# Kernel tuning notes

Measured on AMD Instinct MI355X. Metric: run time of the kernel, lower is better.

## Reference

```python
import jax, jax.numpy as jnp
import numpy as np

N_HEADS = 8
N_POINTS = 4
LN_EPS = 1e-5


def _ln(x, g, b):
    m = jnp.mean(x, -1, keepdims=True)
    v = jnp.mean((x - m) ** 2, -1, keepdims=True)
    return (x - m) * jax.lax.rsqrt(v + LN_EPS) * g + b


def _mha(q, k, v, wq, bq, wk, bk, wv, bv, wo, bo):
    B, Lq, C = q.shape
    Dh = C // N_HEADS
    Q = (q @ wq.T + bq).reshape(B, Lq, N_HEADS, Dh)
    K = (k @ wk.T + bk).reshape(B, -1, N_HEADS, Dh)
    V = (v @ wv.T + bv).reshape(B, -1, N_HEADS, Dh)
    s = jnp.einsum('bqhd,bkhd->bhqk', Q, K) * (1.0 / float(np.sqrt(Dh)))
    a = jax.nn.softmax(s, -1)
    o = jnp.einsum('bhqk,bkhd->bqhd', a, V).reshape(B, Lq, C)
    return o @ wo.T + bo


def _ref_points(h, w, L):
    ry = jnp.linspace(0.5, h - 0.5, h) / h
    rx = jnp.linspace(0.5, w - 0.5, w) / w
    gy, gx = jnp.meshgrid(ry, rx, indexing='ij')
    ref = jnp.stack([gx.reshape(-1), gy.reshape(-1)], -1)[None]  # (1, h*w, 2)
    return jnp.broadcast_to(ref[:, :, None, :], (1, h * w, L, 2))


def _deform_core(value, shapes, starts, loc, aw):
    # value: (B, Len_in, H, Dh); loc: (B, Lq, H, L, P, 2); aw: (B, Lq, H, L, P)
    B, _, H, Dh = value.shape
    Lq, P = loc.shape[1], loc.shape[4]
    out = jnp.zeros((B, H, Lq, Dh), value.dtype)
    for l in range(shapes.shape[0]):
        Hl, Wl = int(shapes[l, 0]), int(shapes[l, 1])
        s = int(starts[l])
        v = value[:, s:s + Hl * Wl].transpose(0, 2, 1, 3)  # (B, H, Hl*Wl, Dh)
        # grid_sample(align_corners=False, padding_mode='zeros') pixel coords
        xl = loc[:, :, :, l, :, 0] * Wl - 0.5  # (B, Lq, H, P)
        yl = loc[:, :, :, l, :, 1] * Hl - 0.5
        x0 = jnp.floor(xl); y0 = jnp.floor(yl)
        fx = xl - x0; fy = yl - y0
        x0 = x0.astype(jnp.int32); y0 = y0.astype(jnp.int32)
        acc = jnp.zeros((B, H, Lq, P, Dh), value.dtype)
        for dy, dx in ((0, 0), (0, 1), (1, 0), (1, 1)):
            xi = x0 + dx; yi = y0 + dy
            wgt = (fx if dx else 1.0 - fx) * (fy if dy else 1.0 - fy)
            valid = ((xi >= 0) & (xi < Wl) & (yi >= 0) & (yi < Hl)).astype(value.dtype)
            idx = (jnp.clip(yi, 0, Hl - 1) * Wl + jnp.clip(xi, 0, Wl - 1))
            idx = idx.transpose(0, 2, 1, 3).reshape(B, H, Lq * P)
            g = jnp.take_along_axis(v, idx[..., None], axis=2).reshape(B, H, Lq, P, Dh)
            acc = acc + g * (wgt * valid).transpose(0, 2, 1, 3)[..., None]
        out = out + jnp.einsum('bhqpd,bqhp->bhqd', acc, aw[:, :, :, l])
    return out.transpose(0, 2, 1, 3).reshape(B, Lq, H * Dh)


def reference(tgt, query_pos, src, wq, bq, wk, bk, wv, bv, wo, bo, ln2_g, ln2_b,
              w_off, b_off, w_attn, b_attn, w_val, b_val, w_cout, b_cout,
              ln1_g, ln1_b, w1, b1, w2, b2, ln3_g, ln3_b,
              src_spatial_shapes, level_start_index, h, w):
    shapes = np.asarray(src_spatial_shapes)
    starts = np.asarray(level_start_index)
    h = int(h); w = int(w)
    L = shapes.shape[0]
    B, Lq, C = tgt.shape
    Dh = C // N_HEADS
    # --- self attention (post-LN residual) ---
    q = tgt + query_pos
    t2 = _mha(q, q, tgt, wq, bq, wk, bk, wv, bv, wo, bo)
    t = _ln(tgt + t2, ln2_g, ln2_b)
    # --- MSDeformAttn cross attention ---
    qc = t + query_pos
    value = (src @ w_val.T + b_val).reshape(B, -1, N_HEADS, Dh)
    off = (qc @ w_off.T + b_off).reshape(B, Lq, N_HEADS, L, N_POINTS, 2)
    aw = (qc @ w_attn.T + b_attn).reshape(B, Lq, N_HEADS, L * N_POINTS)
    aw = jax.nn.softmax(aw, -1).reshape(B, Lq, N_HEADS, L, N_POINTS)
    norm = jnp.stack([shapes[:, 1].astype(np.float32), shapes[:, 0].astype(np.float32)], -1)  # (L,2): (W,H)
    rp = _ref_points(h, w, L)  # (1, Lq, L, 2)
    loc = rp[:, :, None, :, None, :] + off / norm[None, None, None, :, None, :]
    samp = _deform_core(value, shapes, starts, loc, aw)
    t2 = samp @ w_cout.T + b_cout
    t = _ln(t + t2, ln1_g, ln1_b)
    # --- FFN ---
    t2 = jax.nn.relu(t @ w1.T + b1) @ w2.T + b2
    t = _ln(t + t2, ln3_g, ln3_b)
    return t


def setup_inputs() -> dict:
    key = jax.random.key(0)
    B, C, L, P, dff = 2, 256, 4, 4, 1024
    h = w = 48
    shapes = np.array([[48, 48], [24, 24], [12, 12], [6, 6]], np.int32)
    starts = np.array([0, 2304, 2880, 3024], np.int32)
    Len_in = 3060
    Lq = h * w
    ks = iter(jax.random.split(key, 40))
    def rn(shape, s=0.02):
        return jax.random.normal(next(ks), shape, jnp.float32) * s
    return dict(
        tgt=rn((B, Lq, C), 1.0), query_pos=rn((B, Lq, C), 1.0), src=rn((B, Len_in, C), 1.0),
        wq=rn((C, C)), bq=rn((C,)), wk=rn((C, C)), bk=rn((C,)), wv=rn((C, C)), bv=rn((C,)),
        wo=rn((C, C)), bo=rn((C,)),
        ln2_g=jnp.ones((C,)), ln2_b=jnp.zeros((C,)),
        w_off=rn((N_HEADS * L * P * 2, C)), b_off=rn((N_HEADS * L * P * 2,)),
        w_attn=rn((N_HEADS * L * P, C)), b_attn=rn((N_HEADS * L * P,)),
        w_val=rn((C, C)), b_val=rn((C,)), w_cout=rn((C, C)), b_cout=rn((C,)),
        ln1_g=jnp.ones((C,)), ln1_b=jnp.zeros((C,)),
        w1=rn((dff, C)), b1=rn((dff,)), w2=rn((C, dff)), b2=rn((C,)),
        ln3_g=jnp.ones((C,)), ln3_b=jnp.zeros((C,)),
        src_spatial_shapes=shapes, level_start_index=starts, h=h, w=w)
```

## Files before the change

kernel.cpp:

```cpp
#include <hip/hip_runtime.h>
#include <hip/hip_bf16.h>
#include <math.h>

typedef __hip_bfloat16 bf16;
typedef __attribute__((ext_vector_type(8))) short short8;
typedef __attribute__((ext_vector_type(4))) short short4v;
typedef __attribute__((ext_vector_type(4))) float f32x4;

static constexpr int B   = 2;
static constexpr int LQ  = 2304;
static constexpr int C   = 256;
static constexpr int NH  = 8;
static constexpr int DH  = 32;
static constexpr int NL  = 4;
static constexpr int NP  = 4;
static constexpr int LEN = 3060;
static constexpr int DFF = 1024;
static constexpr int MQ  = B * LQ;
static constexpr int MV  = B * LEN;
static constexpr int SZ1 = MQ * C;

#define MFMA16(a, b, c) __builtin_amdgcn_mfma_f32_16x16x32_bf16(a, b, c, 0, 0, 0)

__device__ __forceinline__ float ldf(const void* p, size_t i, int bf) {
  return bf ? __bfloat162float(((const bf16*)p)[i]) : ((const float*)p)[i];
}
__device__ __forceinline__ short fl2s(float v) {
  bf16 h = __float2bfloat16(v);
  return *(short*)&h;
}
__device__ __forceinline__ short fl2s_fast(float v) {
  union { float f; unsigned u; } x; x.f = v;
  return (short)((x.u + 0x8000u) >> 16);
}
__device__ __forceinline__ float s2fl(short s) {
  return __bfloat162float(*(bf16*)&s);
}
__device__ __forceinline__ int wire_is_bf16(const unsigned* gprobe) {
  return gprobe[0] == 0x3F803F80u;
}
__device__ __forceinline__ short8 add2bf(short8 a, short8 b) {
  short8 r;
#pragma unroll
  for (int j = 0; j < 8; ++j) r[j] = fl2s(s2fl(a[j]) + s2fl(b[j]));
  return r;
}

static constexpr int CVN = 20;
__device__ const int g_cvt_cnt[CVN] = {
  65536, 65536, 256, 256, 65536, 256, 65536, 256,
  65536, 32768, 256, 128, 65536, 256, 65536, 256,
  262144, 1024, 262144, 256};
__device__ const int g_cvt_off[CVN] = {
  0, 65536, 131072, 131328, 131584, 197120, 197376, 262912,
  263168, 328704, 361472, 361728, 361856, 427392, 427648, 493184,
  493440, 755584, 756608, 1018752};
static constexpr int CV_WQ = 0, CV_WK = 65536, CV_BQ = 131072, CV_BK = 131328;
static constexpr int CV_WV = 131584, CV_BV = 197120;
static constexpr int CV_WO = 197376, CV_BO = 262912;
static constexpr int CV_WOFF = 263168, CV_WATTN = 328704;
static constexpr int CV_BOFF = 361472, CV_BATTN = 361728;
static constexpr int CV_WVAL = 361856, CV_BVAL = 427392;
static constexpr int CV_WCOUT = 427648, CV_BCOUT = 493184;
static constexpr int CV_W1 = 493440, CV_B1 = 755584;
static constexpr int CV_W2 = 756608, CV_B2 = 1018752;
static constexpr int CV_TOTAL = 1019008;

struct CvtArgs { const void* p[22]; };

__global__ __launch_bounds__(256) void prep_all(CvtArgs a, const void* __restrict__ qpos,
                                                short* __restrict__ cvt,
                                                short* __restrict__ tgt16,
                                                short* __restrict__ q16,
                                                short* __restrict__ src16,
                                                const unsigned* __restrict__ gprobe) {
  if (wire_is_bf16(gprobe)) return;
  const int seg = blockIdx.y;
  const int cnt = (seg < 20) ? g_cvt_cnt[seg] : (seg == 20 ? SZ1 : MV * C);
  const int stride = gridDim.x * 256;
  for (int i = blockIdx.x * 256 + threadIdx.x; i < cnt; i += stride) {
    if (seg < 20) {
      cvt[g_cvt_off[seg] + i] = fl2s(((const float*)a.p[seg])[i]);
    } else if (seg == 20) {
      float t = ((const float*)a.p[20])[i];
      tgt16[i] = fl2s(t);
      q16[i] = fl2s(t + ((const float*)qpos)[i]);
    } else {
      src16[i] = fl2s(((const float*)a.p[21])[i]);
    }
  }
}

struct GemmJob {
  int Xmode;
  const short* Xbf; const void* Xwire; const void* Xwire2;
  const short* Wcvt; const short* bcvt;
  const void* Wwire; const void* bwire;
  void* Y;
  int M, N, K, ldY, col0, relu, out_mode, nblk_x;
  float qscale;
};
struct GemmBatch { GemmJob j[4]; int start[5]; int njobs; };

template <int MR>
__global__ __launch_bounds__(256) void gemm_mfma(GemmBatch nb,
                                                 const unsigned* __restrict__ gprobe) {
  constexpr int MT = MR / 64;
  const int fl = wire_is_bf16(gprobe);
  int id = blockIdx.x;
  int jj = 0;
  while (jj + 1 < nb.njobs && id >= nb.start[jj + 1]) ++jj;
  const GemmJob jb = nb.j[jj];
  const bool qcf = (jb.Xmode == 4) && fl;
  const short* Xsel = jb.Xbf;
  if ((jb.Xmode == 2 || jb.Xmode == 3) && fl) Xsel = (const short*)jb.Xwire;
  const short* Wsel = fl ? (const short*)jb.Wwire : jb.Wcvt;
  const short* bsel = fl ? (const short*)jb.bwire : jb.bcvt;
  const int local = id - nb.start[jj];
  const int bx = local % jb.nblk_x;
  const int by = local / jb.nblk_x;
  const int M = jb.M, N = jb.N, K = jb.K;

  __shared__ short Xs[MR][72];
  __shared__ short Ws[64][72];
  const int tid = threadIdx.x;
  const int wave = tid >> 6, lane = tid & 63;
  const int quad = lane >> 4, l16 = lane & 15;
  const int m0 = bx * MR, n0 = by * 64;
  f32x4 acc[MT][4];
#pragma unroll
  for (int mt = 0; mt < MT; ++mt)
#pragma unroll
    for (int nt = 0; nt < 4; ++nt) acc[mt][nt] = f32x4{0.f, 0.f, 0.f, 0.f};

  const int xrow = (MR == 128) ? (tid >> 1) : (tid >> 2);
  const int xcol = (MR == 128) ? ((tid & 1) * 32) : ((tid & 3) * 16);
  constexpr int XU = (MR == 128) ? 4 : 2;
  const int wrow = tid >> 2;
  const int wcol = (tid & 3) * 16;
  int xr = m0 + xrow; if (xr >= M) xr = M - 1;
  const short* xp = qcf ? nullptr : (Xsel + (size_t)xr * K);
  const short* tp = qcf ? ((const short*)jb.Xwire + (size_t)xr * K) : nullptr;
  const short* pp = qcf ? ((const short*)jb.Xwire2 + (size_t)xr * K) : nullptr;
  const short* wp = Wsel + (size_t)(n0 + wrow) * K;

  for (int k0 = 0; k0 < K; k0 += 64) {
    if (qcf) {
#pragma unroll
      for (int u = 0; u < XU; ++u) {
        short8 t8 = *(const short8*)(tp + k0 + xcol + u * 8);
        short8 p8 = *(const short8*)(pp + k0 + xcol + u * 8);
        *(short8*)&Xs[xrow][xcol + u * 8] = add2bf(t8, p8);
      }
    } else {
#pragma unroll
      for (int u = 0; u < XU; ++u)
        *(short8*)&Xs[xrow][xcol + u * 8] = *(const short8*)(xp + k0 + xcol + u * 8);
    }
    *(short8*)&Ws[wrow][wcol]     = *(const short8*)(wp + k0 + wcol);
    *(short8*)&Ws[wrow][wcol + 8] = *(const short8*)(wp + k0 + wcol + 8);
    __syncthreads();
#pragma unroll
    for (int kc = 0; kc < 2; ++kc) {
#pragma unroll
      for (int mt = 0; mt < MT; ++mt) {
        short8 a = *(const short8*)&Xs[wave * (16 * MT) + mt * 16 + l16][kc * 32 + quad * 8];
#pragma unroll
        for (int nt = 0; nt < 4; ++nt) {
          short8 b = *(const short8*)&Ws[nt * 16 + l16][kc * 32 + quad * 8];
          acc[mt][nt] = MFMA16(a, b, acc[mt][nt]);
        }
      }
    }
    __syncthreads();
  }

  if (jb.out_mode == 2) {
#pragma unroll
    for (int mt = 0; mt < MT; ++mt) {
      const int mbase = m0 + wave * (16 * MT) + mt * 16 + quad * 4;
      const int b = mbase / LQ;
      const int qb_ = mbase - b * LQ;
#pragma unroll
      for (int nt = 0; nt < 4; ++nt) {
        const int n = n0 + nt * 16 + l16;
        const float bv = s2fl(bsel[n]);
        short4v v4;
#pragma unroll
        for (int r = 0; r < 4; ++r) v4[r] = fl2s(acc[mt][nt][r] + bv);
        *(short4v*)((short*)jb.Y + (size_t)(b * 256 + n) * LQ + qb_) = v4;
      }
    }
    return;
  }
#pragma unroll
  for (int mt = 0; mt < MT; ++mt)
#pragma unroll
    for (int nt = 0; nt < 4; ++nt) {
      const int n = n0 + nt * 16 + l16;
      const float bv = s2fl(bsel[n]);
#pragma unroll
      for (int r = 0; r < 4; ++r) {
        const int m = m0 + wave * (16 * MT) + mt * 16 + quad * 4 + r;
        if (m < M) {
          float v = (acc[mt][nt][r] + bv) * jb.qscale;
          if (jb.relu) v = fmaxf(v, 0.f);
          if (jb.out_mode == 1)
            ((short*)jb.Y)[(size_t)m * jb.ldY + jb.col0 + n] = fl2s(v);
          else
            ((float*)jb.Y)[(size_t)m * jb.ldY + jb.col0 + n] = v;
        }
      }
    }
}

__global__ __launch_bounds__(256) void flash_attn(const short* __restrict__ QK,
                                                  const short* __restrict__ Vt,
                                                  short* __restrict__ Op) {
  constexpr int LDQK = 512;
  constexpr int NC = LQ / 64;
  constexpr int NQT = 3;
  const int qb = blockIdx.x;
  const int bh = blockIdx.y;
  const int b = bh >> 3, h = bh & 7;
  const int tid = threadIdx.x;
  const int wave = tid >> 6, lane = tid & 63;
  const int quad = lane >> 4, l16 = lane & 15;

  __shared__ short Ps[4][16][68];
  __shared__ float lsh[256];

  const int q0 = qb * 48;
  const size_t rowb = (size_t)(b * LQ);
  const short* kcol = QK + 256 + h * DH + quad * 8;
  const short* vt0 = Vt + (size_t)(b * 256 + h * 32 + l16) * LQ + quad * 8;
  const short* vt1 = Vt + (size_t)(b * 256 + h * 32 + 16 + l16) * LQ + quad * 8;

  short8 qfrag[NQT];
#pragma unroll
  for (int qt = 0; qt < NQT; ++qt)
    qfrag[qt] = *(const short8*)(QK + (rowb + q0 + qt * 16 + l16) * LDQK + h * DH + quad * 8);

  f32x4 o0[NQT], o1[NQT];
  float lrow[NQT];
#pragma unroll
  for (int qt = 0; qt < NQT; ++qt) {
    o0[qt] = f32x4{0.f, 0.f, 0.f, 0.f};
    o1[qt] = f32x4{0.f, 0.f, 0.f, 0.f};
    lrow[qt] = 0.f;
  }

  short8 kf[4], vf[4];
  {
    const int k0 = wave * 64;
#pragma unroll
    for (int kt = 0; kt < 4; ++kt)
      kf[kt] = *(const short8*)(kcol + (rowb + k0 + kt * 16 + l16) * LDQK);
    vf[0] = *(const short8*)(vt0 + k0);
    vf[1] = *(const short8*)(vt0 + k0 + 32);
    vf[2] = *(const short8*)(vt1 + k0);
    vf[3] = *(const short8*)(vt1 + k0 + 32);
  }

  for (int c = wave; c < NC; c += 4) {
    short8 kn[4], vn[4];
    if (c + 4 < NC) {
      const int k0n = (c + 4) * 64;
#pragma unroll
      for (int kt = 0; kt < 4; ++kt)
        kn[kt] = *(const short8*)(kcol + (rowb + k0n + kt * 16 + l16) * LDQK);
      vn[0] = *(const short8*)(vt0 + k0n);
      vn[1] = *(const short8*)(vt0 + k0n + 32);
      vn[2] = *(const short8*)(vt1 + k0n);
      vn[3] = *(const short8*)(vt1 + k0n + 32);
    }

#pragma unroll
    for (int qt = 0; qt < NQT; ++qt) {
      f32x4 s[4];
#pragma unroll
      for (int kt = 0; kt < 4; ++kt) {
        f32x4 z = {0.f, 0.f, 0.f, 0.f};
        s[kt] = MFMA16(kf[kt], qfrag[qt], z);
      }

      float ps = 0.f;
#pragma unroll
      for (int kt = 0; kt < 4; ++kt)
#pragma unroll
        for (int r = 0; r < 4; ++r) {
          float p = __expf(s[kt][r]);
          s[kt][r] = p;
          ps += p;
        }
      lrow[qt] += ps;

#pragma unroll
      for (int kt = 0; kt < 4; ++kt) {
        short4v pk;
#pragma unroll
        for (int r = 0; r < 4; ++r) pk[r] = fl2s_fast(s[kt][r]);
        *(short4v*)&Ps[wave][l16][kt * 16 + quad * 4] = pk;
      }

#pragma unroll
      for (int half = 0; half < 2; ++half) {
        short4v a0 = *(const short4v*)&Ps[wave][l16][half * 32 + quad * 8];
        short4v a1 = *(const short4v*)&Ps[wave][l16][half * 32 + quad * 8 + 4];
        short8 afrag;
#pragma unroll
        for (int j = 0; j < 4; ++j) { afrag[j] = a0[j]; afrag[4 + j] = a1[j]; }
        o0[qt] = MFMA16(afrag, vf[half], o0[qt]);
        o1[qt] = MFMA16(afrag, vf[2 + half], o1[qt]);
      }
    }

#pragma unroll
    for (int kt = 0; kt < 4; ++kt) { kf[kt] = kn[kt]; vf[kt] = vn[kt]; }
  }

  float* obuf = (float*)&Ps[0][0][0];
  for (int qt = 0; qt < NQT; ++qt) {
    __syncthreads();
    lsh[(wave * 4 + quad) * 16 + l16] = lrow[qt];
#pragma unroll
    for (int r = 0; r < 4; ++r) {
      const int q = quad * 4 + r;
      obuf[(wave * 16 + q) * 32 + l16] = o0[qt][r];
      obuf[(wave * 16 + q) * 32 + 16 + l16] = o1[qt][r];
    }
    __syncthreads();
#pragma unroll
    for (int e = tid; e < 512; e += 256) {
      const int q = e >> 5, d = e & 31;
      float lg = 0.f;
#pragma unroll
      for (int i = 0; i < 16; ++i) lg += lsh[i * 16 + q];
      float ov = 0.f;
#pragma unroll
      for (int w = 0; w < 4; ++w) ov += obuf[(w * 16 + q) * 32 + d];
      Op[(rowb + q0 + qt * 16 + q) * C + h * DH + d] = fl2s_fast(ov / lg);
    }
  }
}

__global__ __launch_bounds__(256) void ln_kern(const void* __restrict__ A, int a_mode,
                                               const float* __restrict__ R,
                                               const void* __restrict__ g,
                                               const void* __restrict__ be,
                                               float* __restrict__ Yf32,
                                               short* __restrict__ Y16,
                                               void* __restrict__ Yfinal,
                                               const void* __restrict__ pos,
                                               short* __restrict__ Yqc,
                                               int rows, const unsigned* __restrict__ gprobe) {
  const int fl = wire_is_bf16(gprobe);
  const int row = blockIdx.x * 4 + (threadIdx.x >> 6);
  const int lane = threadIdx.x & 63;
  if (row >= rows) return;
  float x[4], s = 0.f, s2 = 0.f;
#pragma unroll
  for (int u = 0; u < 4; ++u) {
    int c = lane + 64 * u;
    size_t idx = (size_t)row * C + c;
    float a = (a_mode == 1) ? ldf(A, idx, fl) : ((const float*)A)[idx];
    x[u] = a + R[idx];
    s += x[u];
    s2 += x[u] * x[u];
  }
#pragma unroll
  for (int off = 32; off > 0; off >>= 1) {
    s += __shfl_xor(s, off);
    s2 += __shfl_xor(s2, off);
  }
  const float mean = s * (1.f / C);
  const float var = fmaxf(s2 * (1.f / C) - mean * mean, 0.f);
  const float inv = rsqrtf(var + 1e-5f);
#pragma unroll
  for (int u = 0; u < 4; ++u) {
    int c = lane + 64 * u;
    size_t idx = (size_t)row * C + c;
    float y = (x[u] - mean) * inv * ldf(g, c, fl) + ldf(be, c, fl);
    if (Yfinal) {
      if (fl) ((short*)Yfinal)[idx] = fl2s(y);
      else ((float*)Yfinal)[idx] = y;
    } else {
      if (Yf32) Yf32[idx] = y;
      if (Y16) Y16[idx] = fl2s(y);
      if (Yqc) Yqc[idx] = fl2s(y + ldf(pos, idx, fl));
    }
  }
}

__global__ __launch_bounds__(256) void deform_kern(const short* __restrict__ value,
                                                   const float* __restrict__ oa,
                                                   const int* __restrict__ shapes,
                                                   const int* __restrict__ starts,
                                                   const int* __restrict__ hp,
                                                   const int* __restrict__ wp,
                                                   short* __restrict__ samp) {
  const int bq = blockIdx.x * 4 + (threadIdx.x >> 6);
  const int b = bq / LQ, q = bq % LQ;
  const int lane = threadIdx.x & 63;
  const int h_ = lane >> 3;
  const int d0 = (lane & 7) * 4;

  const int w0 = *wp, h0 = *hp;
  const int qx = q % w0, qy = q / w0;
  const float refx = (qx + 0.5f) / (float)w0;
  const float refy = (qy + 0.5f) / (float)h0;

  const float* offp = oa + (size_t)bq * 384 + h_ * 32;
  const float* awraw = oa + (size_t)bq * 384 + 256 + h_ * 16;

  float e[16];
  float mm = -1e30f;
#pragma unroll
  for (int j = 0; j < 16; ++j) mm = fmaxf(mm, awraw[j]);
  float ssum = 0.f;
#pragma unroll
  for (int j = 0; j < 16; ++j) {
    e[j] = __expf(awraw[j] - mm);
    ssum += e[j];
  }
  const float sinv = 1.f / ssum;

  float acc0 = 0.f, acc1 = 0.f, acc2 = 0.f, acc3 = 0.f;
  for (int l = 0; l < NL; ++l) {
    const int Hl = shapes[l * 2 + 0];
    const int Wl = shapes[l * 2 + 1];
    const int st = starts[l];
    const short* vbase = value + ((size_t)(b * LEN + st)) * C + h_ * DH + d0;
#pragma unroll
    for (int p = 0; p < NP; ++p) {
      const float ox = offp[l * 8 + p * 2 + 0];
      const float oy = offp[l * 8 + p * 2 + 1];
      const float a = e[l * 4 + p] * sinv;
      const float xl = refx * Wl + ox - 0.5f;
      const float yl = refy * Hl + oy - 0.5f;
      const float x0f = floorf(xl), y0f = floorf(yl);
      const float fx = xl - x0f, fy = yl - y0f;
      const int x0 = (int)x0f, y0 = (int)y0f;
#pragma unroll
      for (int corner = 0; corner < 4; ++corner) {
        const int dx = corner & 1, dy = corner >> 1;
        const int xi = x0 + dx, yi = y0 + dy;
        const float wx = dx ? fx : 1.f - fx;
        const float wy = dy ? fy : 1.f - fy;
        const bool valid = (xi >= 0) & (xi < Wl) & (yi >= 0) & (yi < Hl);
        if (valid) {
          const float w = a * wx * wy;
          short4v v4 = *(const short4v*)(vbase + (size_t)(yi * Wl + xi) * C);
          acc0 += w * s2fl(v4[0]);
          acc1 += w * s2fl(v4[1]);
          acc2 += w * s2fl(v4[2]);
          acc3 += w * s2fl(v4[3]);
        }
      }
    }
  }
  short4v out;
  out[0] = fl2s(acc0); out[1] = fl2s(acc1); out[2] = fl2s(acc2); out[3] = fl2s(acc3);
  *(short4v*)(samp + (size_t)bq * C + h_ * DH + d0) = out;
}

extern "C" void kernel_launch(void* const* d_in, const int* in_sizes, int n_in,
                              void* d_out, int out_size, void* d_ws, size_t ws_size,
                              hipStream_t stream) {
  const void* tgt       = d_in[0];
  const void* query_pos = d_in[1];
  const void* src       = d_in[2];
  const void* wq = d_in[3];  const void* bq = d_in[4];
  const void* wk = d_in[5];  const void* bk = d_in[6];
  const void* wv = d_in[7];  const void* bv = d_in[8];
  const void* wo = d_in[9];  const void* bo = d_in[10];
  const void* ln2_g = d_in[11]; const void* ln2_b = d_in[12];
  const void* w_off = d_in[13]; const void* b_off = d_in[14];
  const void* w_attn = d_in[15]; const void* b_attn = d_in[16];
  const void* w_val = d_in[17]; const void* b_val = d_in[18];
  const void* w_cout = d_in[19]; const void* b_cout = d_in[20];
  const void* ln1_g = d_in[21]; const void* ln1_b = d_in[22];
  const void* w1 = d_in[23]; const void* b1 = d_in[24];
  const void* w2 = d_in[25]; const void* b2 = d_in[26];
  const void* ln3_g = d_in[27]; const void* ln3_b = d_in[28];
  const int* shapes = (const int*)d_in[29];
  const int* starts = (const int*)d_in[30];
  const int* hp = (const int*)d_in[31];
  const int* wp = (const int*)d_in[32];
  const unsigned* gprobe = (const unsigned*)ln2_g;

  short* cvt    = (short*)((char*)d_ws + 256);
  short* tgt16  = cvt + CV_TOTAL;
  short* q16    = tgt16 + SZ1;
  short* src16  = q16 + SZ1;
  short* qk_out = src16 + (size_t)MV * C;
  short* vt16   = qk_out + (size_t)MQ * 512;
  short* ao16   = vt16 + SZ1;
  short* valb   = ao16 + SZ1;
  short* ffn1   = valb + (size_t)MV * C;
  short* t1_16  = ffn1 + (size_t)MQ * DFF;
  float* t2a    = (float*)(t1_16 + SZ1);
  float* t_32   = t2a + SZ1;
  float* t1_32  = t_32 + SZ1;
  float* oa     = t1_32 + SZ1;

  const float scale = 1.f / sqrtf((float)DH);
  const dim3 blk(256);
  const int NX128 = MQ / 128;
  const int NX64  = MQ / 64;
  const int NXV   = (MV + 127) / 128;

  CvtArgs ca;
  ca.p[0] = wq;  ca.p[1] = wk;  ca.p[2] = bq;  ca.p[3] = bk;
  ca.p[4] = wv;  ca.p[5] = bv;  ca.p[6] = wo;  ca.p[7] = bo;
  ca.p[8] = w_off; ca.p[9] = w_attn; ca.p[10] = b_off; ca.p[11] = b_attn;
  ca.p[12] = w_val; ca.p[13] = b_val; ca.p[14] = w_cout; ca.p[15] = b_cout;
  ca.p[16] = w1; ca.p[17] = b1; ca.p[18] = w2; ca.p[19] = b2;
  ca.p[20] = tgt; ca.p[21] = src;
  prep_all<<<dim3(96, 22), blk, 0, stream>>>(ca, query_pos, cvt, tgt16, q16, src16, gprobe);

  {
    GemmBatch nb;
    nb.njobs = 4;
    nb.j[0] = {4, q16, tgt, query_pos, cvt + CV_WQ, cvt + CV_BQ, wq, bq, qk_out,
               MQ, 256, 256, 512, 0, 0, 1, NX128, scale};
    nb.j[1] = {4, q16, tgt, query_pos, cvt + CV_WK, cvt + CV_BK, wk, bk, qk_out,
               MQ, 256, 256, 512, 256, 0, 1, NX128, 1.f};
    nb.j[2] = {2, tgt16, tgt, nullptr, cvt + CV_WV, cvt + CV_BV, wv, bv, vt16,
               MQ, 256, 256, 0, 0, 0, 2, NX128, 1.f};
    nb.j[3] = {3, src16, src, nullptr, cvt + CV_WVAL, cvt + CV_BVAL, w_val, b_val, valb,
               MV, 256, 256, 256, 0, 0, 1, NXV, 1.f};
    nb.start[0] = 0;
    nb.start[1] = NX128 * 4;
    nb.start[2] = nb.start[1] + NX128 * 4;
    nb.start[3] = nb.start[2] + NX128 * 4;
    nb.start[4] = nb.start[3] + NXV * 4;
    gemm_mfma<128><<<nb.start[4], blk, 0, stream>>>(nb, gprobe);
  }
  flash_attn<<<dim3(LQ / 48, B * NH), blk, 0, stream>>>(qk_out, vt16, ao16);
  {
    GemmBatch nb;
    nb.njobs = 1;
    nb.j[0] = {0, ao16, nullptr, nullptr, cvt + CV_WO, cvt + CV_BO, wo, bo, t2a,
               MQ, 256, 256, 256, 0, 0, 0, NX64, 1.f};
    nb.start[0] = 0; nb.start[1] = NX64 * 4;
    gemm_mfma<64><<<nb.start[1], blk, 0, stream>>>(nb, gprobe);
  }
  ln_kern<<<MQ / 4, blk, 0, stream>>>(tgt, 1, t2a, ln2_g, ln2_b,
                                      t_32, nullptr, nullptr, query_pos, q16, MQ, gprobe);

  {
    GemmBatch nb;
    nb.njobs = 2;
    nb.j[0] = {0, q16, nullptr, nullptr, cvt + CV_WOFF, cvt + CV_BOFF, w_off, b_off, oa,
               MQ, 256, 256, 384, 0, 0, 0, NX64, 1.f};
    nb.j[1] = {0, q16, nullptr, nullptr, cvt + CV_WATTN, cvt + CV_BATTN, w_attn, b_attn, oa,
               MQ, 128, 256, 384, 256, 0, 0, NX64, 1.f};
    nb.start[0] = 0;
    nb.start[1] = NX64 * 4;
    nb.start[2] = nb.start[1] + NX64 * 2;
    gemm_mfma<64><<<nb.start[2], blk, 0, stream>>>(nb, gprobe);
  }
  deform_kern<<<MQ / 4, blk, 0, stream>>>(valb, oa, shapes, starts, hp, wp, ao16);
  {
    GemmBatch nb;
    nb.njobs = 1;
    nb.j[0] = {0, ao16, nullptr, nullptr, cvt + CV_WCOUT, cvt + CV_BCOUT, w_cout, b_cout, t2a,
               MQ, 256, 256, 256, 0, 0, 0, NX64, 1.f};
    nb.start[0] = 0; nb.start[1] = NX64 * 4;
    gemm_mfma<64><<<nb.start[1], blk, 0, stream>>>(nb, gprobe);
  }
  ln_kern<<<MQ / 4, blk, 0, stream>>>(t_32, 2, t2a, ln1_g, ln1_b,
                                      t1_32, t1_16, nullptr, nullptr, nullptr, MQ, gprobe);

  {
    GemmBatch nb;
    nb.njobs = 1;
    nb.j[0] = {0, t1_16, nullptr, nullptr, cvt + CV_W1, cvt + CV_B1, w1, b1, ffn1,
               MQ, 1024, 256, 1024, 0, 1, 1, NX128, 1.f};
    nb.start[0] = 0; nb.start[1] = NX128 * 16;
    gemm_mfma<128><<<nb.start[1], blk, 0, stream>>>(nb, gprobe);
  }
  {
    GemmBatch nb;
    nb.njobs = 1;
    nb.j[0] = {0, ffn1, nullptr, nullptr, cvt + CV_W2, cvt + CV_B2, w2, b2, t2a,
               MQ, 256, 1024, 256, 0, 0, 0, NX64, 1.f};
    nb.start[0] = 0; nb.start[1] = NX64 * 4;
    gemm_mfma<64><<<nb.start[1], blk, 0, stream>>>(nb, gprobe);
  }
  ln_kern<<<MQ / 4, blk, 0, stream>>>(t1_32, 2, t2a, ln3_g, ln3_b,
                                      nullptr, nullptr, d_out, nullptr, nullptr, MQ, gprobe);
}
```

Baseline: 288.0 us.

## Fuse output-projection GEMMs with residual add and LayerNorm into one kernel

Adds a gemm_ln kernel in which each block computes a full 32x256 output row tile, then adds bias and residual and applies LayerNorm in the epilogue using a cross-wave reduction through shared memory. It replaces the three GEMM+ln_kern pairs (attention out-proj, deformable out-proj, FFN second layer), removing the fp32 intermediate buffer round trip and three kernel launches. The trade-off is that each block now loads the full 256-column weight tile per k-step, giving smaller M tiles, more weight traffic, and lower per-block parallelism and efficiency than the previous GEMM.

```diff
diff --git a/kernel.cpp b/kernel.cpp
--- a/kernel.cpp
+++ b/kernel.cpp
@@ -214,6 +214,133 @@
     }
 }
 
+struct LnGemmArgs {
+  const short* X;
+  const short* Wcvt; const short* bcvt;
+  const void* Wwire; const void* bwire;
+  const void* R; int Rmode;
+  const void* g; const void* be;
+  float* Yf32; short* Y16; void* Yfinal;
+  const void* pos; short* Yqc;
+  int K;
+};
+
+__global__ __launch_bounds__(256) void gemm_ln(LnGemmArgs a,
+                                               const unsigned* __restrict__ gprobe) {
+  const int fl = wire_is_bf16(gprobe);
+  const short* Wsel = fl ? (const short*)a.Wwire : a.Wcvt;
+  const short* bsel = fl ? (const short*)a.bwire : a.bcvt;
+  const int K = a.K;
+
+  __shared__ short Xs[32][72];
+  __shared__ short Ws[256][72];
+  __shared__ float red[4][32][2];
+  __shared__ float minv[32][2];
+
+  const int tid = threadIdx.x;
+  const int wave = tid >> 6, lane = tid & 63;
+  const int quad = lane >> 4, l16 = lane & 15;
+  const int m0 = blockIdx.x * 32;
+
+  f32x4 acc[2][4];
+#pragma unroll
+  for (int mt = 0; mt < 2; ++mt)
+#pragma unroll
+    for (int nt = 0; nt < 4; ++nt) acc[mt][nt] = f32x4{0.f, 0.f, 0.f, 0.f};
+
+  const int xrow = tid >> 3, xcol = (tid & 7) * 8;
+  const int wrow = tid >> 2, wcol = (tid & 3) * 16;
+  const short* xp = a.X + (size_t)(m0 + xrow) * K + xcol;
+
+  for (int k0 = 0; k0 < K; k0 += 64) {
+    *(short8*)&Xs[xrow][xcol] = *(const short8*)(xp + k0);
+#pragma unroll
+    for (int u = 0; u < 4; ++u) {
+      const short* wp = Wsel + (size_t)(u * 64 + wrow) * K + k0 + wcol;
+      *(short8*)&Ws[u * 64 + wrow][wcol]     = *(const short8*)(wp);
+      *(short8*)&Ws[u * 64 + wrow][wcol + 8] = *(const short8*)(wp + 8);
+    }
+    __syncthreads();
+#pragma unroll
+    for (int kc = 0; kc < 2; ++kc)
+#pragma unroll
+      for (int mt = 0; mt < 2; ++mt) {
+        short8 av = *(const short8*)&Xs[mt * 16 + l16][kc * 32 + quad * 8];
+#pragma unroll
+        for (int nt = 0; nt < 4; ++nt) {
+          short8 bv = *(const short8*)&Ws[wave * 64 + nt * 16 + l16][kc * 32 + quad * 8];
+          acc[mt][nt] = MFMA16(av, bv, acc[mt][nt]);
+        }
+      }
+    __syncthreads();
+  }
+
+  float gc[4], bc[4], bb[4];
+#pragma unroll
+  for (int nt = 0; nt < 4; ++nt) {
+    const int n = wave * 64 + nt * 16 + l16;
+    gc[nt] = ldf(a.g, n, fl);
+    bc[nt] = ldf(a.be, n, fl);
+    bb[nt] = s2fl(bsel[n]);
+  }
+#pragma unroll
+  for (int mt = 0; mt < 2; ++mt)
+#pragma unroll
+    for (int r = 0; r < 4; ++r) {
+      const int rloc = mt * 16 + quad * 4 + r;
+      const size_t row = (size_t)(m0 + rloc);
+      float s = 0.f, s2 = 0.f;
+#pragma unroll
+      for (int nt = 0; nt < 4; ++nt) {
+        const int n = wave * 64 + nt * 16 + l16;
+        const size_t idx = row * C + n;
+        const float rv = (a.Rmode == 1) ? ldf(a.R, idx, fl) : ((const float*)a.R)[idx];
+        const float v = acc[mt][nt][r] + bb[nt] + rv;
+        acc[mt][nt][r] = v;
+        s += v;
+        s2 += v * v;
+      }
+#pragma unroll
+      for (int off = 8; off > 0; off >>= 1) {
+        s  += __shfl_xor(s, off);
+        s2 += __shfl_xor(s2, off);
+      }
+      if (l16 == 0) { red[wave][rloc][0] = s; red[wave][rloc][1] = s2; }
+    }
+  __syncthreads();
+  if (tid < 32) {
+    const float s  = red[0][tid][0] + red[1][tid][0] + red[2][tid][0] + red[3][tid][0];
+    const float s2 = red[0][tid][1] + red[1][tid][1] + red[2][tid][1] + red[3][tid][1];
+    const float mean = s * (1.f / C);
+    const float var = fmaxf(s2 * (1.f / C) - mean * mean, 0.f);
+    minv[tid][0] = mean;
+    minv[tid][1] = rsqrtf(var + 1e-5f);
+  }
+  __syncthreads();
+#pragma unroll
+  for (int mt = 0; mt < 2; ++mt)
+#pragma unroll
+    for (int r = 0; r < 4; ++r) {
+      const int rloc = mt * 16 + quad * 4 + r;
+      const size_t row = (size_t)(m0 + rloc);
+      const float mean = minv[rloc][0], inv = minv[rloc][1];
+#pragma unroll
+      for (int nt = 0; nt < 4; ++nt) {
+        const int n = wave * 64 + nt * 16 + l16;
+        const size_t idx = row * C + n;
+        const float y = (acc[mt][nt][r] - mean) * inv * gc[nt] + bc[nt];
+        if (a.Yfinal) {
+          if (fl) ((short*)a.Yfinal)[idx] = fl2s(y);
+          else    ((float*)a.Yfinal)[idx] = y;
+        } else {
+          if (a.Yf32) a.Yf32[idx] = y;
+          if (a.Y16)  a.Y16[idx] = fl2s(y);
+          if (a.Yqc)  a.Yqc[idx] = fl2s(y + ldf(a.pos, idx, fl));
+        }
+      }
+    }
+}
+
 __global__ __launch_bounds__(256) void flash_attn(const short* __restrict__ QK,
                                                   const short* __restrict__ Vt,
                                                   short* __restrict__ Op) {
@@ -340,54 +467,6 @@
 #pragma unroll
       for (int w = 0; w < 4; ++w) ov += obuf[(w * 16 + q) * 32 + d];
       Op[(rowb + q0 + qt * 16 + q) * C + h * DH + d] = fl2s_fast(ov / lg);
-    }
-  }
-}
-
-__global__ __launch_bounds__(256) void ln_kern(const void* __restrict__ A, int a_mode,
-                                               const float* __restrict__ R,
-                                               const void* __restrict__ g,
-                                               const void* __restrict__ be,
-                                               float* __restrict__ Yf32,
-                                               short* __restrict__ Y16,
-                                               void* __restrict__ Yfinal,
-                                               const void* __restrict__ pos,
-                                               short* __restrict__ Yqc,
-                                               int rows, const unsigned* __restrict__ gprobe) {
-  const int fl = wire_is_bf16(gprobe);
-  const int row = blockIdx.x * 4 + (threadIdx.x >> 6);
-  const int lane = threadIdx.x & 63;
-  if (row >= rows) return;
-  float x[4], s = 0.f, s2 = 0.f;
-#pragma unroll
-  for (int u = 0; u < 4; ++u) {
-    int c = lane + 64 * u;
-    size_t idx = (size_t)row * C + c;
-    float a = (a_mode == 1) ? ldf(A, idx, fl) : ((const float*)A)[idx];
-    x[u] = a + R[idx];
-    s += x[u];
-    s2 += x[u] * x[u];
-  }
-#pragma unroll
-  for (int off = 32; off > 0; off >>= 1) {
-    s += __shfl_xor(s, off);
-    s2 += __shfl_xor(s2, off);
-  }
-  const float mean = s * (1.f / C);
-  const float var = fmaxf(s2 * (1.f / C) - mean * mean, 0.f);
-  const float inv = rsqrtf(var + 1e-5f);
-#pragma unroll
-  for (int u = 0; u < 4; ++u) {
-    int c = lane + 64 * u;
-    size_t idx = (size_t)row * C + c;
-    float y = (x[u] - mean) * inv * ldf(g, c, fl) + ldf(be, c, fl);
-    if (Yfinal) {
-      if (fl) ((short*)Yfinal)[idx] = fl2s(y);
-      else ((float*)Yfinal)[idx] = y;
-    } else {
-      if (Yf32) Yf32[idx] = y;
-      if (Y16) Y16[idx] = fl2s(y);
-      if (Yqc) Yqc[idx] = fl2s(y + ldf(pos, idx, fl));
     }
   }
 }
@@ -499,8 +578,7 @@
   short* valb   = ao16 + SZ1;
   short* ffn1   = valb + (size_t)MV * C;
   short* t1_16  = ffn1 + (size_t)MQ * DFF;
-  float* t2a    = (float*)(t1_16 + SZ1);
-  float* t_32   = t2a + SZ1;
+  float* t_32   = (float*)(t1_16 + SZ1);
   float* t1_32  = t_32 + SZ1;
   float* oa     = t1_32 + SZ1;
 
@@ -508,6 +586,7 @@
   const dim3 blk(256);
   const int NX128 = MQ / 128;
   const int NX64  = MQ / 64;
+  const int NX32  = MQ / 32;
   const int NXV   = (MV + 127) / 128;
 
   CvtArgs ca;
@@ -538,16 +617,16 @@
     gemm_mfma<128><<<nb.start[4], blk, 0, stream>>>(nb, gprobe);
   }
   flash_attn<<<dim3(LQ / 48, B * NH), blk, 0, stream>>>(qk_out, vt16, ao16);
+
   {
-    GemmBatch nb;
-    nb.njobs = 1;
-    nb.j[0] = {0, ao16, nullptr, nullptr, cvt + CV_WO, cvt + CV_BO, wo, bo, t2a,
-               MQ, 256, 256, 256, 0, 0, 0, NX64, 1.f};
-    nb.start[0] = 0; nb.start[1] = NX64 * 4;
-    gemm_mfma<64><<<nb.start[1], blk, 0, stream>>>(nb, gprobe);
-  }
-  ln_kern<<<MQ / 4, blk, 0, stream>>>(tgt, 1, t2a, ln2_g, ln2_b,
-                                      t_32, nullptr, nullptr, query_pos, q16, MQ, gprobe);
+    LnGemmArgs a;
+    a.X = ao16; a.Wcvt = cvt + CV_WO; a.bcvt = cvt + CV_BO; a.Wwire = wo; a.bwire = bo;
+    a.R = tgt; a.Rmode = 1; a.g = ln2_g; a.be = ln2_b;
+    a.Yf32 = t_32; a.Y16 = nullptr; a.Yfinal = nullptr;
+    a.pos = query_pos; a.Yqc = q16;
+    a.K = 256;
+    gemm_ln<<<NX32, blk, 0, stream>>>(a, gprobe);
+  }
 
   {
     GemmBatch nb;
@@ -562,16 +641,16 @@
     gemm_mfma<64><<<nb.start[2], blk, 0, stream>>>(nb, gprobe);
   }
   deform_kern<<<MQ / 4, blk, 0, stream>>>(valb, oa, shapes, starts, hp, wp, ao16);
+
   {
-    GemmBatch nb;
-    nb.njobs = 1;
-    nb.j[0] = {0, ao16, nullptr, nullptr, cvt + CV_WCOUT, cvt + CV_BCOUT, w_cout, b_cout, t2a,
-               MQ, 256, 256, 256, 0, 0, 0, NX64, 1.f};
-    nb.start[0] = 0; nb.start[1] = NX64 * 4;
-    gemm_mfma<64><<<nb.start[1], blk, 0, stream>>>(nb, gprobe);
-  }
-  ln_kern<<<MQ / 4, blk, 0, stream>>>(t_32, 2, t2a, ln1_g, ln1_b,
-                                      t1_32, t1_16, nullptr, nullptr, nullptr, MQ, gprobe);
+    LnGemmArgs a;
+    a.X = ao16; a.Wcvt = cvt + CV_WCOUT; a.bcvt = cvt + CV_BCOUT; a.Wwire = w_cout; a.bwire = b_cout;
+    a.R = t_32; a.Rmode = 2; a.g = ln1_g; a.be = ln1_b;
+    a.Yf32 = t1_32; a.Y16 = t1_16; a.Yfinal = nullptr;
+    a.pos = nullptr; a.Yqc = nullptr;
+    a.K = 256;
+    gemm_ln<<<NX32, blk, 0, stream>>>(a, gprobe);
+  }
 
   {
     GemmBatch nb;
@@ -582,13 +661,12 @@
     gemm_mfma<128><<<nb.start[1], blk, 0, stream>>>(nb, gprobe);
   }
   {
-    GemmBatch nb;
-    nb.njobs = 1;
-    nb.j[0] = {0, ffn1, nullptr, nullptr, cvt + CV_W2, cvt + CV_B2, w2, b2, t2a,
-               MQ, 256, 1024, 256, 0, 0, 0, NX64, 1.f};
-    nb.start[0] = 0; nb.start[1] = NX64 * 4;
-    gemm_mfma<64><<<nb.start[1], blk, 0, stream>>>(nb, gprobe);
-  }
-  ln_kern<<<MQ / 4, blk, 0, stream>>>(t1_32, 2, t2a, ln3_g, ln3_b,
-                                      nullptr, nullptr, d_out, nullptr, nullptr, MQ, gprobe);
-}
+    LnGemmArgs a;
+    a.X = ffn1; a.Wcvt = cvt + CV_W2; a.bcvt = cvt + CV_B2; a.Wwire = w2; a.bwire = b2;
+    a.R = t1_32; a.Rmode = 2; a.g = ln3_g; a.be = ln3_b;
+    a.Yf32 = nullptr; a.Y16 = nullptr; a.Yfinal = d_out;
+    a.pos = nullptr; a.Yqc = nullptr;
+    a.K = 1024;
+    gemm_ln<<<NX32, blk, 0, stream>>>(a, gprobe);
+  }
+}
```

New measurement: 290.5 us. No clear change (+0.9%).
